# Optimization experiments

Hardware: AMD Instinct MI355X
Metric: run time of the kernel (lower is better)

The kernel has to match this reference:

```python
import jax, jax.numpy as jnp
import numpy as np

NEG_INF = -9e15  # matches torch's -9000000000000000.0 mask value


def setup_inputs() -> dict:
    key = jax.random.key(0)
    k1, k2, k3, k4 = jax.random.split(key, 4)
    B, F_in, T, N, F_out = 8, 64, 12, 512, 64
    inp = {
        "input": jax.random.normal(k1, (B, F_in, T, N), dtype=jnp.float32),
        "adj": jax.random.randint(k2, (B, T, N, N), 0, 2, dtype=jnp.int32),
        "W": jax.random.normal(k3, (F_in, F_out), dtype=jnp.float32),
        "a": jax.random.normal(k4, (2 * F_out, 1), dtype=jnp.float32),
    }
    return inp


def reference(input, adj, W, a):
    # input: [B, F_in, T, N], adj: [B, T, N, N]
    F_out = W.shape[1]
    x = jnp.transpose(input, (0, 2, 3, 1))          # [B, T, N, F_in]
    Wh = jnp.einsum('btnf,fo->btno', x, W)          # [B, T, N, F_out]
    # score decomposition: e[i,j] = leakyrelu(a1.Wh_i + a2.Wh_j)
    a1 = a[:F_out, 0]
    a2 = a[F_out:, 0]
    f1 = Wh @ a1                                    # [B, T, N]
    f2 = Wh @ a2                                    # [B, T, N]
    e = jax.nn.leaky_relu(f1[..., :, None] + f2[..., None, :], 0.2)
    e = jnp.where(adj > 0, e, NEG_INF)
    attn = jax.nn.softmax(e, axis=-1)               # [B, T, N, N]
    h = jnp.einsum('btij,btjo->btio', attn, Wh)     # [B, T, N, F_out]
    return jax.nn.elu(h)                            # concat=True -> elu
```

## Files before the change

### kernel.cpp

```cpp
#include <hip/hip_runtime.h>
#include <hip/hip_bf16.h>

typedef float fx4 __attribute__((ext_vector_type(4)));
typedef short i16x8 __attribute__((ext_vector_type(8)));
typedef unsigned short u16;

#define NEG_INF_F (-9.0e15f)

__device__ inline u16 f2bf(float v){
  __hip_bfloat16 h = __float2bfloat16(v);
  return *reinterpret_cast<u16*>(&h);
}
__device__ inline unsigned pk2(float lo, float hi){
  return (unsigned)f2bf(lo) | ((unsigned)f2bf(hi) << 16);
}

__global__ __launch_bounds__(256) void gat_pre(
    const float* __restrict__ input,
    const float* __restrict__ W,
    const float* __restrict__ Avec,
    const int*   __restrict__ adj,
    u16*      __restrict__ whB,
    float*    __restrict__ f1w,
    float*    __restrict__ f2w,
    unsigned* __restrict__ maskw)
{
  __shared__ float Wl[64*64];
  __shared__ float Al[128];
  __shared__ u16   Rp[16384];
  const int bid = blockIdx.x;
  const int tid = threadIdx.x;

  if (bid >= 192) {
    const int t = (bid - 192) * 256 + tid;
    const uint4* src = (const uint4*)adj + (size_t)t * 8;
    uint4 v[8];
    #pragma unroll
    for (int i = 0; i < 8; ++i) v[i] = src[i];
    unsigned m = 0u;
    #pragma unroll
    for (int i = 0; i < 8; ++i) {
      if ((int)v[i].x > 0) m |= 1u << (4*i+0);
      if ((int)v[i].y > 0) m |= 1u << (4*i+1);
      if ((int)v[i].z > 0) m |= 1u << (4*i+2);
      if ((int)v[i].w > 0) m |= 1u << (4*i+3);
    }
    maskw[t] = m;
    return;
  }

  const int bt = bid >> 1, xb = bid & 1;
  const int b  = bt / 12, t = bt % 12;
  const int n  = xb * 256 + tid;

  {
    const fx4* src = (const fx4*)W;
    fx4* dst = (fx4*)Wl;
    #pragma unroll
    for (int i = 0; i < 4; ++i) dst[tid + 256*i] = src[tid + 256*i];
    if (tid < 32) ((fx4*)Al)[tid] = ((const fx4*)Avec)[tid];
  }
  __syncthreads();

  const float* xp = input + ((size_t)b*64*12 + t) * 512 + n;

  fx4 acc[16];
  #pragma unroll
  for (int i = 0; i < 16; ++i) acc[i] = (fx4){0.f,0.f,0.f,0.f};

  #pragma unroll 8
  for (int f = 0; f < 64; ++f) {
    float xv = xp[(size_t)f * 6144];
    const fx4* wr = (const fx4*)(Wl + f*64);
    #pragma unroll
    for (int o4 = 0; o4 < 16; ++o4) acc[o4] += xv * wr[o4];
  }

  float s1 = 0.f, s2 = 0.f;
  #pragma unroll
  for (int o4 = 0; o4 < 16; ++o4) {
    fx4 v  = acc[o4];
    fx4 w1 = ((const fx4*)Al)[o4];
    fx4 w2 = ((const fx4*)Al)[o4 + 16];
    s1 += v[0]*w1[0] + v[1]*w1[1] + v[2]*w1[2] + v[3]*w1[3];
    s2 += v[0]*w2[0] + v[1]*w2[1] + v[2]*w2[2] + v[3]*w2[3];
  }
  f1w[bt*512 + n] = s1;
  f2w[bt*512 + n] = s2;

  const int ktl  = (n >> 5) & 7;
  const int q    = (n >> 3) & 3;
  const int e    = n & 7;
  const int rowb = ktl*2048 + q*128 + e;
  #pragma unroll
  for (int o4 = 0; o4 < 16; ++o4) {
    #pragma unroll
    for (int c = 0; c < 4; ++c) {
      const int o = o4*4 + c;
      Rp[rowb + (o >> 4)*512 + (o & 15)*8] = f2bf(acc[o4][c]);
    }
  }
  __syncthreads();

  uint4* dst = (uint4*)(whB + ((size_t)bt*16 + xb*8) * 2048);
  const uint4* src = (const uint4*)Rp;
  #pragma unroll
  for (int i = 0; i < 8; ++i) dst[tid + 256*i] = src[tid + 256*i];
}

__global__ __launch_bounds__(256, 4) void gat_attn(
    const unsigned* __restrict__ maskw,
    const u16*   __restrict__ whB,
    const float* __restrict__ f1w,
    const float* __restrict__ f2w,
    float*       __restrict__ out)
{
  __shared__ float f1l[16];
  __shared__ float wmaxl[4];
  __shared__ float sums[16];
  __shared__ unsigned maskl[16][16];
  __shared__ uint2 lutl[16];
  __shared__ u16   attnl[16*512];

  const int tid = threadIdx.x;
  const int l   = tid & 63;
  const int w   = tid >> 6;
  const int bt  = blockIdx.y;
  const int it  = blockIdx.x;

  ((unsigned*)maskl)[tid] = maskw[((size_t)bt*512 + it*16)*16 + tid];
  if (tid < 16) f1l[tid] = f1w[bt*512 + it*16 + tid];
  if (tid < 16) {
    const unsigned nb = tid;
    lutl[tid] = (uint2){ ((nb&1u)?0xFFFFu:0u) | ((nb&2u)?0xFFFF0000u:0u),
                         ((nb&4u)?0xFFFFu:0u) | ((nb&8u)?0xFFFF0000u:0u) };
  }
  const float* f2p = f2w + bt*512;
  const fx4 f20 = ((const fx4*)f2p)[l];
  const fx4 f21 = ((const fx4*)f2p)[64 + l];
  float m2 = fmaxf(fmaxf(fmaxf(f20[0], f20[1]), fmaxf(f20[2], f20[3])),
                   fmaxf(fmaxf(f21[0], f21[1]), fmaxf(f21[2], f21[3])));
  #pragma unroll
  for (int off = 32; off >= 1; off >>= 1) m2 = fmaxf(m2, __shfl_xor(m2, off));
  if (l == 0) wmaxl[w] = m2;
  __syncthreads();
  const float F2max = fmaxf(fmaxf(wmaxl[0], wmaxl[1]), fmaxf(wmaxl[2], wmaxl[3]));

  fx4 v0, v1, vh0, vh1;
  #pragma unroll
  for (int c = 0; c < 4; ++c) {
    v0[c]  = __expf(f20[c] - F2max);
    v1[c]  = __expf(f21[c] - F2max);
    vh0[c] = __expf(0.2f*(f20[c] - F2max));
    vh1[c] = __expf(0.2f*(f21[c] - F2max));
  }
  const float thrBig = F2max - 80.f;
  const unsigned big_lo = (f20[0] > thrBig ? 1u : 0u) | (f20[1] > thrBig ? 2u : 0u)
                        | (f20[2] > thrBig ? 4u : 0u) | (f20[3] > thrBig ? 8u : 0u);
  const unsigned big_hi = (f21[0] > thrBig ? 1u : 0u) | (f21[1] > thrBig ? 2u : 0u)
                        | (f21[2] > thrBig ? 4u : 0u) | (f21[3] > thrBig ? 8u : 0u);

  const int R0 = w * 4;
  const int wi = l >> 3;
  const int sh = (l & 7) * 4;

  #pragma unroll
  for (int r = 0; r < 4; ++r) {
    const int rowR = R0 + r;
    const unsigned nib0 = (maskl[rowR][wi]     >> sh) & 0xFu;
    const unsigned nib1 = (maskl[rowR][8 + wi] >> sh) & 0xFu;
    const float f1v = f1l[rowR];

    unsigned w0, w1, w2, w3;
    const unsigned sb = (nib0 & big_lo) | (nib1 & big_hi);
    if (__builtin_expect(__any((int)sb), 1)) {
      const float tR = f1v + F2max;
      const float M  = fmaxf(tR, 0.2f*tR);
      const float u  = __expf(tR - M);
      const float uh = __expf(0.2f*tR - M);
      fx4 PA, PB;
      #pragma unroll
      for (int c = 0; c < 4; ++c) {
        PA[c] = fmaxf(u*v0[c], uh*vh0[c]);
        PB[c] = fmaxf(u*v1[c], uh*vh1[c]);
      }
      const uint2 mA = lutl[nib0];
      const uint2 mB = lutl[nib1];
      w0 = pk2(PA[0], PA[1]) & mA.x;
      w1 = pk2(PA[2], PA[3]) & mA.y;
      w2 = pk2(PB[0], PB[1]) & mB.x;
      w3 = pk2(PB[2], PB[3]) & mB.y;
    } else {
      float mx = NEG_INF_F;
      mx = fmaxf(mx, (nib0 & 1u) ? f20[0] : NEG_INF_F);
      mx = fmaxf(mx, (nib0 & 2u) ? f20[1] : NEG_INF_F);
      mx = fmaxf(mx, (nib0 & 4u) ? f20[2] : NEG_INF_F);
      mx = fmaxf(mx, (nib0 & 8u) ? f20[3] : NEG_INF_F);
      mx = fmaxf(mx, (nib1 & 1u) ? f21[0] : NEG_INF_F);
      mx = fmaxf(mx, (nib1 & 2u) ? f21[1] : NEG_INF_F);
      mx = fmaxf(mx, (nib1 & 4u) ? f21[2] : NEG_INF_F);
      mx = fmaxf(mx, (nib1 & 8u) ? f21[3] : NEG_INF_F);
      #pragma unroll
      for (int off = 32; off >= 1; off >>= 1) mx = fmaxf(mx, __shfl_xor(mx, off));
      const float tM = f1v + mx;
      const float Mc = fmaxf(tM, 0.2f*tM);
      const float Mf = (mx == NEG_INF_F) ? NEG_INF_F : Mc;
      float pv[8];
#define GAT_S(idx, bb_, ff) { float s = f1v + (ff); float lr = fmaxf(s, 0.2f*s); \
      float ee = (bb_) ? lr : NEG_INF_F; pv[idx] = __expf(ee - Mf); }
      GAT_S(0, nib0 & 1u, f20[0]) GAT_S(1, nib0 & 2u, f20[1])
      GAT_S(2, nib0 & 4u, f20[2]) GAT_S(3, nib0 & 8u, f20[3])
      GAT_S(4, nib1 & 1u, f21[0]) GAT_S(5, nib1 & 2u, f21[1])
      GAT_S(6, nib1 & 4u, f21[2]) GAT_S(7, nib1 & 8u, f21[3])
#undef GAT_S
      w0 = pk2(pv[0], pv[1]); w1 = pk2(pv[2], pv[3]);
      w2 = pk2(pv[4], pv[5]); w3 = pk2(pv[6], pv[7]);
    }

    const unsigned swz = (unsigned)((rowR & 7) << 4);
    char* base = (char*)attnl + rowR * 1024;
    *(uint2*)(base + (((unsigned)(      8*l)) ^ swz)) = (uint2){w0, w1};
    *(uint2*)(base + (((unsigned)(512 + 8*l)) ^ swz)) = (uint2){w2, w3};
  }
  __syncthreads();

  const int r = l & 15, q = l >> 4;
  const unsigned swzB = (unsigned)((r & 7) << 4);
  const char* aBase = (const char*)attnl + r * 1024;
  const u16*  wp    = whB + (size_t)bt*32768 + w*512 + l*8;
  i16x8 bones;
  #pragma unroll
  for (int e = 0; e < 8; ++e) bones[e] = (short)0x3F80;
  fx4 acc = {0,0,0,0}, accS = {0,0,0,0};

  #pragma unroll
  for (int kt = 0; kt < 16; ++kt) {
    i16x8 af = *(const i16x8*)(aBase + (((unsigned)(kt*64 + q*16)) ^ swzB));
    i16x8 bf = *(const i16x8*)(wp + kt*2048);
    acc = __builtin_amdgcn_mfma_f32_16x16x32_bf16(af, bf, acc, 0, 0, 0);
    if (w == 0)
      accS = __builtin_amdgcn_mfma_f32_16x16x32_bf16(af, bones, accS, 0, 0, 0);
  }
  if (w == 0 && r == 0) {
    #pragma unroll
    for (int rr = 0; rr < 4; ++rr) sums[q*4 + rr] = accS[rr];
  }
  __syncthreads();

  float* op = out + ((size_t)bt*512 + it*16) * 64;
  #pragma unroll
  for (int rr = 0; rr < 4; ++rr) {
    const float rs = 1.0f / sums[q*4 + rr];
    float v = acc[rr] * rs;
    v = v > 0.f ? v : expm1f(v);
    op[(q*4 + rr)*64 + w*16 + r] = v;
  }
}

extern "C" void kernel_launch(void* const* d_in, const int* in_sizes, int n_in,
                              void* d_out, int out_size, void* d_ws, size_t ws_size,
                              hipStream_t stream) {
  const float* input = (const float*)d_in[0];
  const int*   adj   = (const int*)  d_in[1];
  const float* W     = (const float*)d_in[2];
  const float* Avec  = (const float*)d_in[3];
  float* out = (float*)d_out;

  char* ws = (char*)d_ws;
  u16*      whB   = (u16*)ws;
  float*    f1w   = (float*)(ws + 6291456);
  float*    f2w   = (float*)(ws + 6291456 + 196608);
  unsigned* maskw = (unsigned*)(ws + 6291456 + 393216);

  gat_pre<<<192 + 3072, 256, 0, stream>>>(input, W, Avec, adj,
                                          whB, f1w, f2w, maskw);
  gat_attn<<<dim3(32, 96), 256, 0, stream>>>(maskw, whB, f1w, f2w, out);
}
```

Measured before the change: 51.35 us.

## Fuse adjacency mask packing into attention kernel, dropping intermediate bitmask buffer

Moves conversion of the int adjacency matrix into 4-bit nibbles from the preprocessing kernel into the attention kernel, which loads its 16x512 adj tile directly into shared memory as per-nibble bytes. This removes the global write and re-read of the packed mask and shrinks the prep launch to the projection work only. The attention kernel now carries the full adjacency read and more shared memory, which may affect latency hiding and occupancy.

```diff
diff --git a/kernel.cpp b/kernel.cpp
--- a/kernel.cpp
+++ b/kernel.cpp
@@ -15,43 +15,22 @@
   return (unsigned)f2bf(lo) | ((unsigned)f2bf(hi) << 16);
 }
 
-__global__ __launch_bounds__(256) void gat_pre(
+__global__ __launch_bounds__(256) void gat_prep(
     const float* __restrict__ input,
     const float* __restrict__ W,
     const float* __restrict__ Avec,
-    const int*   __restrict__ adj,
-    u16*      __restrict__ whB,
-    float*    __restrict__ f1w,
-    float*    __restrict__ f2w,
-    unsigned* __restrict__ maskw)
+    u16*   __restrict__ whB,
+    float* __restrict__ f1w,
+    float* __restrict__ f2w)
 {
   __shared__ float Wl[64*64];
   __shared__ float Al[128];
   __shared__ u16   Rp[16384];
-  const int bid = blockIdx.x;
   const int tid = threadIdx.x;
-
-  if (bid >= 192) {
-    const int t = (bid - 192) * 256 + tid;
-    const uint4* src = (const uint4*)adj + (size_t)t * 8;
-    uint4 v[8];
-    #pragma unroll
-    for (int i = 0; i < 8; ++i) v[i] = src[i];
-    unsigned m = 0u;
-    #pragma unroll
-    for (int i = 0; i < 8; ++i) {
-      if ((int)v[i].x > 0) m |= 1u << (4*i+0);
-      if ((int)v[i].y > 0) m |= 1u << (4*i+1);
-      if ((int)v[i].z > 0) m |= 1u << (4*i+2);
-      if ((int)v[i].w > 0) m |= 1u << (4*i+3);
-    }
-    maskw[t] = m;
-    return;
-  }
-
-  const int bt = bid >> 1, xb = bid & 1;
-  const int b  = bt / 12, t = bt % 12;
-  const int n  = xb * 256 + tid;
+  const int bt  = blockIdx.y;
+  const int b   = bt / 12, t = bt % 12;
+  const int xb  = blockIdx.x;
+  const int n   = xb * 256 + tid;
 
   {
     const fx4* src = (const fx4*)W;
@@ -109,7 +88,7 @@
 }
 
 __global__ __launch_bounds__(256, 4) void gat_attn(
-    const unsigned* __restrict__ maskw,
+    const int*   __restrict__ adj,
     const u16*   __restrict__ whB,
     const float* __restrict__ f1w,
     const float* __restrict__ f2w,
@@ -118,7 +97,7 @@
   __shared__ float f1l[16];
   __shared__ float wmaxl[4];
   __shared__ float sums[16];
-  __shared__ unsigned maskl[16][16];
+  __shared__ unsigned char masknib[2048];
   __shared__ uint2 lutl[16];
   __shared__ u16   attnl[16*512];
 
@@ -128,21 +107,35 @@
   const int bt  = blockIdx.y;
   const int it  = blockIdx.x;
 
-  ((unsigned*)maskl)[tid] = maskw[((size_t)bt*512 + it*16)*16 + tid];
+  const uint4* adjblk = (const uint4*)(adj + ((size_t)bt*512 + it*16)*512);
+  uint4 av[8];
+  #pragma unroll
+  for (int i = 0; i < 8; ++i) av[i] = adjblk[tid + 256*i];
+
+  const float* f2p = f2w + bt*512;
+  const fx4 f20 = ((const fx4*)f2p)[l];
+  const fx4 f21 = ((const fx4*)f2p)[64 + l];
   if (tid < 16) f1l[tid] = f1w[bt*512 + it*16 + tid];
   if (tid < 16) {
     const unsigned nb = tid;
     lutl[tid] = (uint2){ ((nb&1u)?0xFFFFu:0u) | ((nb&2u)?0xFFFF0000u:0u),
                          ((nb&4u)?0xFFFFu:0u) | ((nb&8u)?0xFFFF0000u:0u) };
   }
-  const float* f2p = f2w + bt*512;
-  const fx4 f20 = ((const fx4*)f2p)[l];
-  const fx4 f21 = ((const fx4*)f2p)[64 + l];
   float m2 = fmaxf(fmaxf(fmaxf(f20[0], f20[1]), fmaxf(f20[2], f20[3])),
                    fmaxf(fmaxf(f21[0], f21[1]), fmaxf(f21[2], f21[3])));
   #pragma unroll
   for (int off = 32; off >= 1; off >>= 1) m2 = fmaxf(m2, __shfl_xor(m2, off));
   if (l == 0) wmaxl[w] = m2;
+
+  #pragma unroll
+  for (int i = 0; i < 8; ++i) {
+    unsigned nb = 0u;
+    if ((int)av[i].x > 0) nb |= 1u;
+    if ((int)av[i].y > 0) nb |= 2u;
+    if ((int)av[i].z > 0) nb |= 4u;
+    if ((int)av[i].w > 0) nb |= 8u;
+    masknib[tid + 256*i] = (unsigned char)nb;
+  }
   __syncthreads();
   const float F2max = fmaxf(fmaxf(wmaxl[0], wmaxl[1]), fmaxf(wmaxl[2], wmaxl[3]));
 
@@ -161,14 +154,12 @@
                         | (f21[2] > thrBig ? 4u : 0u) | (f21[3] > thrBig ? 8u : 0u);
 
   const int R0 = w * 4;
-  const int wi = l >> 3;
-  const int sh = (l & 7) * 4;
 
   #pragma unroll
   for (int r = 0; r < 4; ++r) {
     const int rowR = R0 + r;
-    const unsigned nib0 = (maskl[rowR][wi]     >> sh) & 0xFu;
-    const unsigned nib1 = (maskl[rowR][8 + wi] >> sh) & 0xFu;
+    const unsigned nib0 = masknib[rowR*128 + l];
+    const unsigned nib1 = masknib[rowR*128 + 64 + l];
     const float f1v = f1l[rowR];
 
     unsigned w0, w1, w2, w3;
@@ -267,12 +258,10 @@
   float* out = (float*)d_out;
 
   char* ws = (char*)d_ws;
-  u16*      whB   = (u16*)ws;
-  float*    f1w   = (float*)(ws + 6291456);
-  float*    f2w   = (float*)(ws + 6291456 + 196608);
-  unsigned* maskw = (unsigned*)(ws + 6291456 + 393216);
-
-  gat_pre<<<192 + 3072, 256, 0, stream>>>(input, W, Avec, adj,
-                                          whB, f1w, f2w, maskw);
-  gat_attn<<<dim3(32, 96), 256, 0, stream>>>(maskw, whB, f1w, f2w, out);
-}
+  u16*   whB = (u16*)ws;
+  float* f1w = (float*)(ws + 6291456);
+  float* f2w = (float*)(ws + 6291456 + 196608);
+
+  gat_prep<<<dim3(2, 96), 256, 0, stream>>>(input, W, Avec, whB, f1w, f2w);
+  gat_attn<<<dim3(32, 96), 256, 0, stream>>>(adj, whB, f1w, f2w, out);
+}
```

Result: slower. 53.66 us (+4.5%).
